# Optimization experiments

Hardware: AMD Instinct MI355X
Metric: run time of the kernel (lower is better)

The kernel has to match this reference:

```python
import jax, jax.numpy as jnp
import numpy as np

INC = 64; OUTC = 64; TS = 3; CS = 3; MAXN = 10; SIGMA = 2.0; STRIDE = 1
TAU = 0.1


def _gaussian_decay(length, max_val, sigma):
    x = np.arange(length, dtype=np.float32)
    y = max_val * np.exp(-x ** 2 / (2.0 * sigma ** 2))
    return (np.floor(y) + 1).astype(np.int64)


def _get_p_n(t_size, c_size, max_number, sigma):
    f_num = _gaussian_decay(t_size, max_number, sigma)
    c_num = _gaussian_decay(c_size, max_number, sigma)
    px, py = [], []
    for i in range(1, t_size):
        for _ in range(int(f_num[i])):
            px.append(0); py.append(i)
    for i in range(c_size):
        for _ in range(int(c_num[i])):
            px.append(i); py.append(0)
    f_number = int(f_num.sum()) - max_number - 1 if t_size > 0 else 0
    for i in range(c_size):
        for j in range(c_size):
            px.append(i); py.append(j)
    p_n = np.stack([np.array(px, np.float32), np.array(py, np.float32)], 0)  # (2, N)
    return p_n, f_number, p_n.shape[1] - f_number


def _conv(x, w, b, groups=1, pad=0):
    y = jax.lax.conv_general_dilated(
        x, w, (1, 1), [(pad, pad), (pad, pad)],
        dimension_numbers=('NCHW', 'OIHW', 'NCHW'), feature_group_count=groups)
    return y + b[None, :, None, None]


def _bilinear_sample_zeros(img, coords):
    # img (b,c,H,W); coords (b,N,h,w,2) pixel-space (x,y); zeros padding, align_corners=True
    b, c, H, W = img.shape
    x = coords[..., 0]; y = coords[..., 1]
    x0 = jnp.floor(x); y0 = jnp.floor(y)
    wx1 = x - x0; wy1 = y - y0

    def gather(yi, xi, wgt):
        valid = (xi >= 0) & (xi <= W - 1) & (yi >= 0) & (yi <= H - 1)
        xc = jnp.clip(xi, 0, W - 1).astype(jnp.int32)
        yc = jnp.clip(yi, 0, H - 1).astype(jnp.int32)
        vals = jax.vmap(lambda im, yy, xx: im[:, yy, xx])(img, yc, xc)  # (b,c,N,h,w)
        return vals * (wgt * valid.astype(img.dtype))[:, None]

    return (gather(y0, x0, (1 - wy1) * (1 - wx1)) + gather(y0, x0 + 1, (1 - wy1) * wx1)
            + gather(y0 + 1, x0, wy1 * (1 - wx1)) + gather(y0 + 1, x0 + 1, wy1 * wx1))


def setup_inputs() -> dict:
    key = jax.random.key(0)
    ks = jax.random.split(key, 12)
    p_n_np, f_num, c_num = _get_p_n(TS, CS, MAXN, SIGMA)
    N = p_n_np.shape[1]  # 52
    B, H, W = 4, 64, 64
    s = 0.05
    return {
        'x': jax.random.normal(ks[0], (B, INC, H, W), jnp.float32),
        'p_n': jnp.asarray(p_n_np),
        'dwf_w': jax.random.normal(ks[1], (INC, 1, 3, 3), jnp.float32) * s,
        'dwf_b': jnp.zeros((INC,), jnp.float32),
        'pwf_w': jax.random.normal(ks[2], (2 * f_num, INC, 1, 1), jnp.float32) * s,
        'pwf_b': jnp.zeros((2 * f_num,), jnp.float32),
        'dwc_w': jax.random.normal(ks[3], (INC, 1, 3, 3), jnp.float32) * s,
        'dwc_b': jnp.zeros((INC,), jnp.float32),
        'pwc_w': jax.random.normal(ks[4], (2 * c_num, INC, 1, 1), jnp.float32) * s,
        'pwc_b': jnp.zeros((2 * c_num,), jnp.float32),
        'dwm_w': jax.random.normal(ks[5], (INC, 1, 3, 3), jnp.float32) * s,
        'dwm_b': jnp.zeros((INC,), jnp.float32),
        'pwm_w': jax.random.normal(ks[6], (N + 1, INC, 1, 1), jnp.float32) * s,
        'pwm_b': jnp.zeros((N + 1,), jnp.float32),
        'pc_w': jax.random.normal(ks[7], (OUTC, INC, 1, 1), jnp.float32) * s,
        'pc_b': jnp.zeros((OUTC,), jnp.float32),
        'mlp_w1': jax.random.normal(ks[8], (OUTC, OUTC), jnp.float32) * s,
        'mlp_b1': jnp.zeros((OUTC,), jnp.float32),
        'mlp_w2': jax.random.normal(ks[9], (OUTC, OUTC), jnp.float32) * s,
        'mlp_b2': jnp.zeros((OUTC,), jnp.float32),
    }


def reference(x, p_n, dwf_w, dwf_b, pwf_w, pwf_b, dwc_w, dwc_b, pwc_w, pwc_b,
              dwm_w, dwm_b, pwm_w, pwm_b, pc_w, pc_b, mlp_w1, mlp_b1, mlp_w2, mlp_b2):
    b, c, H, W = x.shape
    N = p_n.shape[1]
    # learned per-pixel offsets (depthwise 3x3 + pointwise 1x1), concat f then c branch
    off_f = _conv(_conv(x, dwf_w, dwf_b, groups=c, pad=1), pwf_w, pwf_b)
    off_c = _conv(_conv(x, dwc_w, dwc_b, groups=c, pad=1), pwc_w, pwc_b)
    offset = jnp.concatenate([off_f, off_c], axis=1)  # (b, 2N, h, w)
    h, w = offset.shape[2], offset.shape[3]
    # modulation scores with learned sparsity threshold
    m = _conv(_conv(x, dwm_w, dwm_b, groups=c, pad=1), pwm_w, pwm_b)  # (b, N+1, h, w)
    sparsity = m[:, -1:]
    scores = m[:, :N]
    soft_mask = jax.nn.sigmoid((scores - sparsity) / TAU)
    mod = jax.nn.softmax(scores + jnp.log(soft_mask + 1e-10), axis=1)  # (b,N,h,w)
    # absolute sampling coordinates: base grid + fixed pattern p_n + learned offset
    dt = x.dtype
    gy, gx = jnp.meshgrid(jnp.arange(0, h * STRIDE, STRIDE, dtype=dt),
                          jnp.arange(0, w * STRIDE, STRIDE, dtype=dt), indexing='ij')
    grid = jnp.stack([gx, gy], -1)[None, None]            # (1,1,h,w,2)
    pn = p_n.T[None, :, None, None, :]                    # (1,N,1,1,2)
    off = offset.reshape(b, 2, N, h, w).transpose(0, 2, 3, 4, 1)  # (b,N,h,w,2)
    abs_c = grid + pn + off
    # normalize to [-1,1] then back to pixel space (grid_sample align_corners=True)
    nx = 2.0 * abs_c[..., 0] / (W - 1) - 1.0
    ny = 2.0 * abs_c[..., 1] / (H - 1) - 1.0
    coords = jnp.stack([(nx + 1.0) * 0.5 * (W - 1), (ny + 1.0) * 0.5 * (H - 1)], -1)
    sampled = _bilinear_sample_zeros(jax.lax.stop_gradient(x), coords)  # (b,c,N,h,w)
    agg = jnp.einsum('bcnhw,bnhw->bchw', sampled, mod)
    out = _conv(agg, pc_w, pc_b)  # 1x1 pointwise conv -> (b,outc,h,w)
    # per-pixel MLP over channels
    h1 = jax.nn.relu(jnp.einsum('bchw,dc->bdhw', out, mlp_w1) + mlp_b1[None, :, None, None])
    h2 = jnp.einsum('bchw,dc->bdhw', h1, mlp_w2) + mlp_b2[None, :, None, None]
    return h2 + x
```

## Files before the change

### kernel.cpp

```cpp
#include <hip/hip_runtime.h>
#include <hip/hip_fp16.h>
#include <cmath>

#define BB 4
#define HH 64
#define WW 64

#define OFFW  9960
#define SBW   13392
#define CMAP  15247
#define FLBC  16072
#define FLB   16073
#define POOLW 18377
#define WIN_H 0
#define TF_H  12240
#define TC_H  14800
#define TM_H  17360
#define AGG_H 34194
#define PCB_H 19920
#define H1_H  22480

typedef _Float16 f16x8 __attribute__((ext_vector_type(8)));
typedef float    f32x4 __attribute__((ext_vector_type(4)));

__global__ __launch_bounds__(256) void transpose_half(const float* __restrict__ x,
                                                      __half* __restrict__ xth) {
    int bid = blockIdx.x;
    int b = bid >> 6, y = bid & 63;
    __shared__ float tile[64][65];
    const float* xp = x + ((size_t)b * 64 * HH + y) * WW;
    #pragma unroll
    for (int k = 0; k < 16; ++k) {
        int idx = threadIdx.x + (k << 8);
        int c = idx >> 6, w = idx & 63;
        tile[c][w] = xp[(size_t)c * HH * WW + w];
    }
    __syncthreads();
    __half* op = xth + ((size_t)(b * HH + y) * WW) * 64;
    #pragma unroll
    for (int k = 0; k < 16; ++k) {
        int idx = threadIdx.x + (k << 8);
        int w = idx >> 6, c = idx & 63;
        op[(size_t)w * 64 + c] = __float2half(tile[c][w]);
    }
}

__device__ inline f32x4 tile_gemm64(const __half* PH, int actH,
                                    const float* __restrict__ W,
                                    const float* __restrict__ Bv,
                                    int m_t, int n_t, int lane) {
    const int row = m_t * 16 + (lane & 15);
    const int kg  = (lane >> 4) * 8;
    const float* wr = W + row * 64 + kg;
    float4 wa0 = *reinterpret_cast<const float4*>(wr);
    float4 wa1 = *reinterpret_cast<const float4*>(wr + 4);
    float4 wb0 = *reinterpret_cast<const float4*>(wr + 32);
    float4 wb1 = *reinterpret_cast<const float4*>(wr + 36);
    f16x8 a0, a1;
    a0[0]=(_Float16)wa0.x; a0[1]=(_Float16)wa0.y; a0[2]=(_Float16)wa0.z; a0[3]=(_Float16)wa0.w;
    a0[4]=(_Float16)wa1.x; a0[5]=(_Float16)wa1.y; a0[6]=(_Float16)wa1.z; a0[7]=(_Float16)wa1.w;
    a1[0]=(_Float16)wb0.x; a1[1]=(_Float16)wb0.y; a1[2]=(_Float16)wb0.z; a1[3]=(_Float16)wb0.w;
    a1[4]=(_Float16)wb1.x; a1[5]=(_Float16)wb1.y; a1[6]=(_Float16)wb1.z; a1[7]=(_Float16)wb1.w;
    const int px = n_t * 16 + (lane & 15);
    f16x8 b0 = *reinterpret_cast<const f16x8*>(&PH[actH + px * 80 + kg]);
    f16x8 b1 = *reinterpret_cast<const f16x8*>(&PH[actH + px * 80 + 32 + kg]);
    f32x4 d;
    const int r0 = m_t * 16 + ((lane >> 4) << 2);
    #pragma unroll
    for (int r = 0; r < 4; ++r) d[r] = Bv[r0 + r];
    d = __builtin_amdgcn_mfma_f32_16x16x32_f16(a0, b0, d, 0, 0, 0);
    d = __builtin_amdgcn_mfma_f32_16x16x32_f16(a1, b1, d, 0, 0, 0);
    return d;
}

__global__ __launch_bounds__(512, 4) void crossd_main(
    const __half* __restrict__ xth, const float* __restrict__ x,
    const float* __restrict__ p_n,
    const float* __restrict__ dwf_w, const float* __restrict__ dwf_b,
    const float* __restrict__ pwf_w, const float* __restrict__ pwf_b,
    const float* __restrict__ dwc_w, const float* __restrict__ dwc_b,
    const float* __restrict__ pwc_w, const float* __restrict__ pwc_b,
    const float* __restrict__ dwm_w, const float* __restrict__ dwm_b,
    const float* __restrict__ pwm_w, const float* __restrict__ pwm_b,
    const float* __restrict__ pc_w, const float* __restrict__ pc_b,
    const float* __restrict__ w1, const float* __restrict__ b1,
    const float* __restrict__ w2, const float* __restrict__ b2,
    float* __restrict__ out)
{
    __shared__ float P[POOLW];
    uint32_t* PU = reinterpret_cast<uint32_t*>(P);
    __half*   PH = reinterpret_cast<__half*>(P);
    const int tid  = threadIdx.x;
    const int lane = tid & 63;
    const int wv   = __builtin_amdgcn_readfirstlane(tid >> 6);
    const int bid = blockIdx.x;
    const int xh = bid & 1, y = (bid >> 1) & 63, b = bid >> 7;
    const int x0 = xh << 5;
    const int ry0 = min(max(y - 1, 0), 59);
    const __half* xbh = xth + (size_t)b * (HH * WW * 64);
    const uint2* xb2 = reinterpret_cast<const uint2*>(xbh);

    {
        for (int idx = tid; idx < 5 * 36 * 16; idx += 512) {
            int j = idx / 576;
            int rem = idx - j * 576;
            int col = rem >> 4, c4v = idx & 15;
            int gcol = min(max(x0 - 1 + col, 0), 63);
            *reinterpret_cast<uint2*>(&PH[(j * 36 + col) * 68 + c4v * 4]) =
                xb2[(((ry0 + j) << 6) + gcol) * 16 + c4v];
        }
        for (int i = tid; i < 25 * 33 + 1; i += 512) P[CMAP + i] = 0.0f;
    }
    __syncthreads();

    {
        const int c = lane;
        float wf9[9], wc9[9], wm9[9];
        #pragma unroll
        for (int k9 = 0; k9 < 9; ++k9) {
            wf9[k9] = dwf_w[c * 9 + k9];
            wc9[k9] = dwc_w[c * 9 + k9];
            wm9[k9] = dwm_w[c * 9 + k9];
        }
        const float bf = dwf_b[c], bc = dwc_b[c], bm = dwm_b[c];
        #pragma unroll
        for (int i = 0; i < 4; ++i) {
            const int pl = wv * 4 + i;
            const int pg = x0 + pl;
            float af = bf, ac = bc, am = bm;
            #pragma unroll
            for (int dy = 0; dy < 3; ++dy) {
                int yy = y + dy - 1;
                if (yy < 0 || yy >= HH) continue;
                int j = yy - ry0;
                #pragma unroll
                for (int dx = 0; dx < 3; ++dx) {
                    int xx = pg + dx - 1;
                    if (xx < 0 || xx >= WW) continue;
                    int co = xx - x0 + 1;
                    float v = __half2float(PH[(j * 36 + co) * 68 + c]);
                    int k = dy * 3 + dx;
                    af = fmaf(v, wf9[k], af);
                    ac = fmaf(v, wc9[k], ac);
                    am = fmaf(v, wm9[k], am);
                }
            }
            PH[TF_H + pl * 80 + c] = __float2half(af);
            PH[TC_H + pl * 80 + c] = __float2half(ac);
            PH[TM_H + pl * 80 + c] = __float2half(am);
        }
    }
    __syncthreads();

    {
        const int n_t = wv & 1;
        const int g   = wv >> 1;
        #pragma unroll
        for (int t = 0; t < 3; ++t) {
            const int m_t = g + t * 4;
            if (m_t < 11) {
                const float *Wb, *Bvb; int rows, actH, r0b, br;
                if (m_t < 2)      { Wb=pwf_w; Bvb=pwf_b; rows=32; actH=TF_H; r0b=m_t*16;     br=0; }
                else if (m_t < 7) { Wb=pwc_w; Bvb=pwc_b; rows=72; actH=TC_H; r0b=(m_t-2)*16; br=1; }
                else              { Wb=pwm_w; Bvb=pwm_b; rows=53; actH=TM_H; r0b=(m_t-7)*16; br=2; }
                const int rl  = min(r0b + (lane & 15), rows - 1);
                const int kg  = (lane >> 4) * 8;
                const float* wr = Wb + rl * 64 + kg;
                float4 wa0 = *reinterpret_cast<const float4*>(wr);
                float4 wa1 = *reinterpret_cast<const float4*>(wr + 4);
                float4 wb0 = *reinterpret_cast<const float4*>(wr + 32);
                float4 wb1 = *reinterpret_cast<const float4*>(wr + 36);
                f16x8 a0, a1;
                a0[0]=(_Float16)wa0.x; a0[1]=(_Float16)wa0.y; a0[2]=(_Float16)wa0.z; a0[3]=(_Float16)wa0.w;
                a0[4]=(_Float16)wa1.x; a0[5]=(_Float16)wa1.y; a0[6]=(_Float16)wa1.z; a0[7]=(_Float16)wa1.w;
                a1[0]=(_Float16)wb0.x; a1[1]=(_Float16)wb0.y; a1[2]=(_Float16)wb0.z; a1[3]=(_Float16)wb0.w;
                a1[4]=(_Float16)wb1.x; a1[5]=(_Float16)wb1.y; a1[6]=(_Float16)wb1.z; a1[7]=(_Float16)wb1.w;
                const int px = n_t * 16 + (lane & 15);
                f16x8 b0 = *reinterpret_cast<const f16x8*>(&PH[actH + px * 80 + kg]);
                f16x8 b1 = *reinterpret_cast<const f16x8*>(&PH[actH + px * 80 + 32 + kg]);
                f32x4 d;
                const int rr0 = r0b + ((lane >> 4) << 2);
                #pragma unroll
                for (int r = 0; r < 4; ++r) d[r] = Bvb[min(rr0 + r, rows - 1)];
                d = __builtin_amdgcn_mfma_f32_16x16x32_f16(a0, b0, d, 0, 0, 0);
                d = __builtin_amdgcn_mfma_f32_16x16x32_f16(a1, b1, d, 0, 0, 0);
                #pragma unroll
                for (int r = 0; r < 4; ++r) {
                    const int rb = rr0 + r;
                    if (rb < rows) {
                        const float v = d[r];
                        if (br == 2)      P[SBW + rb * 35 + px] = v;
                        else {
                            int og = (br == 0) ? rb : 32 + rb;
                            P[OFFW + og * 33 + px] = v;
                        }
                    }
                }
            }
        }
    }
    __syncthreads();

    #pragma unroll 1
    for (int i = 0; i < 4; ++i) {
        const int pl = wv * 4 + i;
        const float sp = P[SBW + 52 * 35 + pl];
        float z = -1e30f;
        if (lane < 52) {
            float s  = P[SBW + lane * 35 + pl];
            float sg = 1.0f / (1.0f + __expf(-(s - sp) * 10.0f));
            z = s + __logf(sg + 1e-10f);
        }
        float mx = z;
        #pragma unroll
        for (int d = 32; d >= 1; d >>= 1) mx = fmaxf(mx, __shfl_xor(mx, d));
        float e = (lane < 52) ? __expf(z - mx) : 0.0f;
        float sm = e;
        #pragma unroll
        for (int d = 32; d >= 1; d >>= 1) sm += __shfl_xor(sm, d);
        if (lane < 52) {
            const float mo = e / sm;
            const int pg = x0 + pl;
            float sx = (float)pg + p_n[lane]      + P[OFFW + lane * 33 + pl];
            float sy = (float)y  + p_n[52 + lane] + P[OFFW + (52 + lane) * 33 + pl];
            float x0f = floorf(sx), y0f = floorf(sy);
            float wx1 = sx - x0f, wy1 = sy - y0f;
            float wx0 = 1.0f - wx1, wy0 = 1.0f - wy1;
            int xi = (int)x0f, yi = (int)y0f;
            bool vx0 = (xi >= 0)  & (xi <= 63);
            bool vx1 = (xi >= -1) & (xi <= 62);
            bool vy0 = (yi >= 0)  & (yi <= 63);
            bool vy1 = (yi >= -1) & (yi <= 62);
            float m00 = (vy0 & vx0) ? mo * wy0 * wx0 : 0.0f;
            float m01 = (vy0 & vx1) ? mo * wy0 * wx1 : 0.0f;
            float m10 = (vy1 & vx0) ? mo * wy1 * wx0 : 0.0f;
            float m11 = (vy1 & vx1) ? mo * wy1 * wx1 : 0.0f;
            const int i0 = xi - pg + 1, j0 = yi - ry0;
            #define PUSH(m, jj, ii, gx, gy) \
                if (m != 0.0f) { \
                    if ((jj) >= 0 && (jj) <= 4 && (ii) >= 0 && (ii) <= 4) { \
                        atomicAdd(&P[CMAP + ((jj) * 5 + (ii)) * 33 + pl], m); \
                    } else { \
                        uint32_t a = (uint32_t)((gy) * 64 + (gx)); \
                        uint32_t sl = atomicAdd(&PU[FLBC], 1u); \
                        if (sl < 512u) { \
                            PU[FLB + sl * 2]     = a | ((uint32_t)pl << 16); \
                            PU[FLB + sl * 2 + 1] = __float_as_uint(m); \
                        } \
                    } \
                }
            PUSH(m00, j0,     i0,     xi,     yi);
            PUSH(m01, j0,     i0 + 1, xi + 1, yi);
            PUSH(m10, j0 + 1, i0,     xi,     yi + 1);
            PUSH(m11, j0 + 1, i0 + 1, xi + 1, yi + 1);
            #undef PUSH
        }
    }
    __syncthreads();

    {
        const int sub = lane >> 4;
        const int c4  = lane & 15;
        const int spx = wv * 4 + sub;
        const int spg = x0 + spx;
        int co[5];
        #pragma unroll
        for (int i = 0; i < 5; ++i) co[i] = min(max(spg - 1 + i, 0), 63) - x0 + 1;
        float4 agg = make_float4(0.f, 0.f, 0.f, 0.f);
        #pragma unroll
        for (int j = 0; j < 5; ++j) {
            #pragma unroll
            for (int i = 0; i < 5; ++i) {
                float w = P[CMAP + (j * 5 + i) * 33 + spx];
                uint2 u = *reinterpret_cast<const uint2*>(&PH[(j * 36 + co[i]) * 68 + c4 * 4]);
                __half2 hlo = *reinterpret_cast<const __half2*>(&u.x);
                __half2 hhi = *reinterpret_cast<const __half2*>(&u.y);
                float2 flo = __half22float2(hlo), fhi = __half22float2(hhi);
                agg.x = fmaf(w, flo.x, agg.x); agg.y = fmaf(w, flo.y, agg.y);
                agg.z = fmaf(w, fhi.x, agg.z); agg.w = fmaf(w, fhi.y, agg.w);
            }
        }
        const int cnt = min((int)PU[FLBC], 512);
        for (int e = 0; e < cnt; ++e) {
            uint32_t ea = PU[FLB + e * 2];
            float m = __uint_as_float(PU[FLB + e * 2 + 1]);
            if ((int)(ea >> 16) == spx) {
                uint2 u = xb2[(ea & 0xFFFFu) * 16 + c4];
                __half2 hlo = *reinterpret_cast<const __half2*>(&u.x);
                __half2 hhi = *reinterpret_cast<const __half2*>(&u.y);
                float2 flo = __half22float2(hlo), fhi = __half22float2(hhi);
                agg.x = fmaf(m, flo.x, agg.x); agg.y = fmaf(m, flo.y, agg.y);
                agg.z = fmaf(m, fhi.x, agg.z); agg.w = fmaf(m, fhi.y, agg.w);
            }
        }
        __half2 p0 = __floats2half2_rn(agg.x, agg.y);
        __half2 p1 = __floats2half2_rn(agg.z, agg.w);
        uint2 pk2;
        pk2.x = *reinterpret_cast<uint32_t*>(&p0);
        pk2.y = *reinterpret_cast<uint32_t*>(&p1);
        *reinterpret_cast<uint2*>(&PH[AGG_H + spx * 80 + c4 * 4]) = pk2;
    }
    __syncthreads();

    {
        f32x4 d = tile_gemm64(PH, AGG_H, pc_w, pc_b, wv >> 1, wv & 1, lane);
        const int px = (wv & 1) * 16 + (lane & 15);
        const int o0 = (wv >> 1) * 16 + ((lane >> 4) << 2);
        __half2 p0 = __floats2half2_rn(d[0], d[1]);
        __half2 p1 = __floats2half2_rn(d[2], d[3]);
        uint2 pk2;
        pk2.x = *reinterpret_cast<uint32_t*>(&p0);
        pk2.y = *reinterpret_cast<uint32_t*>(&p1);
        *reinterpret_cast<uint2*>(&PH[PCB_H + px * 80 + o0]) = pk2;
    }
    __syncthreads();

    {
        f32x4 d = tile_gemm64(PH, PCB_H, w1, b1, wv >> 1, wv & 1, lane);
        #pragma unroll
        for (int r = 0; r < 4; ++r) d[r] = fmaxf(d[r], 0.0f);
        const int px = (wv & 1) * 16 + (lane & 15);
        const int o0 = (wv >> 1) * 16 + ((lane >> 4) << 2);
        __half2 p0 = __floats2half2_rn(d[0], d[1]);
        __half2 p1 = __floats2half2_rn(d[2], d[3]);
        uint2 pk2;
        pk2.x = *reinterpret_cast<uint32_t*>(&p0);
        pk2.y = *reinterpret_cast<uint32_t*>(&p1);
        *reinterpret_cast<uint2*>(&PH[H1_H + px * 80 + o0]) = pk2;
    }
    __syncthreads();

    {
        f32x4 d = tile_gemm64(PH, H1_H, w2, b2, wv >> 1, wv & 1, lane);
        const int px = (wv & 1) * 16 + (lane & 15);
        const int o0 = (wv >> 1) * 16 + ((lane >> 4) << 2);
        #pragma unroll
        for (int r = 0; r < 4; ++r) {
            const int o = o0 + r;
            size_t idx = (((size_t)b * 64 + o) * 64 + y) * 64 + x0 + px;
            out[idx] = d[r] + x[idx];
        }
    }
}

extern "C" void kernel_launch(void* const* d_in, const int* in_sizes, int n_in,
                              void* d_out, int out_size, void* d_ws, size_t ws_size,
                              hipStream_t stream) {
    const float* x     = (const float*)d_in[0];
    const float* p_n   = (const float*)d_in[1];
    const float* dwf_w = (const float*)d_in[2];
    const float* dwf_b = (const float*)d_in[3];
    const float* pwf_w = (const float*)d_in[4];
    const float* pwf_b = (const float*)d_in[5];
    const float* dwc_w = (const float*)d_in[6];
    const float* dwc_b = (const float*)d_in[7];
    const float* pwc_w = (const float*)d_in[8];
    const float* pwc_b = (const float*)d_in[9];
    const float* dwm_w = (const float*)d_in[10];
    const float* dwm_b = (const float*)d_in[11];
    const float* pwm_w = (const float*)d_in[12];
    const float* pwm_b = (const float*)d_in[13];
    const float* pc_w  = (const float*)d_in[14];
    const float* pc_b  = (const float*)d_in[15];
    const float* w1    = (const float*)d_in[16];
    const float* b1    = (const float*)d_in[17];
    const float* w2    = (const float*)d_in[18];
    const float* b2    = (const float*)d_in[19];

    __half* xth = (__half*)d_ws;
    float* outp = (float*)d_out;

    hipLaunchKernelGGL(transpose_half, dim3(BB * HH), dim3(256), 0, stream, x, xth);
    hipLaunchKernelGGL(crossd_main, dim3(BB * HH * 2), dim3(512), 0, stream,
                       xth, x, p_n,
                       dwf_w, dwf_b, pwf_w, pwf_b,
                       dwc_w, dwc_b, pwc_w, pwc_b,
                       dwm_w, dwm_b, pwm_w, pwm_b,
                       pc_w, pc_b, w1, b1, w2, b2, outp);
}
```

Before: 48.83 us.

## Drop separate transpose kernel; load NCHW fp32 input directly into shared tile

Removes the pre-pass kernel that transposed x into a channels-last fp16 workspace. The main kernel now reads the NCHW fp32 input directly, converting to fp16 as it fills the shared halo tile, and the fallback far-sample path reads four strided fp32 channel values. This saves one kernel launch and a full write and read of the transposed tensor. In exchange the halo load makes scalar 4-byte reads with less vectorisation, and far samples now hit four separate cache lines per pixel instead of one 8-byte chunk.

```diff
diff --git a/kernel.cpp b/kernel.cpp
--- a/kernel.cpp
+++ b/kernel.cpp
@@ -22,28 +22,6 @@
 
 typedef _Float16 f16x8 __attribute__((ext_vector_type(8)));
 typedef float    f32x4 __attribute__((ext_vector_type(4)));
-
-__global__ __launch_bounds__(256) void transpose_half(const float* __restrict__ x,
-                                                      __half* __restrict__ xth) {
-    int bid = blockIdx.x;
-    int b = bid >> 6, y = bid & 63;
-    __shared__ float tile[64][65];
-    const float* xp = x + ((size_t)b * 64 * HH + y) * WW;
-    #pragma unroll
-    for (int k = 0; k < 16; ++k) {
-        int idx = threadIdx.x + (k << 8);
-        int c = idx >> 6, w = idx & 63;
-        tile[c][w] = xp[(size_t)c * HH * WW + w];
-    }
-    __syncthreads();
-    __half* op = xth + ((size_t)(b * HH + y) * WW) * 64;
-    #pragma unroll
-    for (int k = 0; k < 16; ++k) {
-        int idx = threadIdx.x + (k << 8);
-        int w = idx >> 6, c = idx & 63;
-        op[(size_t)w * 64 + c] = __float2half(tile[c][w]);
-    }
-}
 
 __device__ inline f32x4 tile_gemm64(const __half* PH, int actH,
                                     const float* __restrict__ W,
@@ -74,7 +52,7 @@
 }
 
 __global__ __launch_bounds__(512, 4) void crossd_main(
-    const __half* __restrict__ xth, const float* __restrict__ x,
+    const float* __restrict__ x,
     const float* __restrict__ p_n,
     const float* __restrict__ dwf_w, const float* __restrict__ dwf_b,
     const float* __restrict__ pwf_w, const float* __restrict__ pwf_b,
@@ -97,17 +75,17 @@
     const int xh = bid & 1, y = (bid >> 1) & 63, b = bid >> 7;
     const int x0 = xh << 5;
     const int ry0 = min(max(y - 1, 0), 59);
-    const __half* xbh = xth + (size_t)b * (HH * WW * 64);
-    const uint2* xb2 = reinterpret_cast<const uint2*>(xbh);
-
-    {
-        for (int idx = tid; idx < 5 * 36 * 16; idx += 512) {
-            int j = idx / 576;
-            int rem = idx - j * 576;
-            int col = rem >> 4, c4v = idx & 15;
+    const float* xb = x + (size_t)b * (64 * HH * WW);
+
+    {
+        for (int idx = tid; idx < 5 * 64 * 36; idx += 512) {
+            int j   = idx / (64 * 36);
+            int rem = idx - j * (64 * 36);
+            int c   = rem / 36;
+            int col = rem - c * 36;
             int gcol = min(max(x0 - 1 + col, 0), 63);
-            *reinterpret_cast<uint2*>(&PH[(j * 36 + col) * 68 + c4v * 4]) =
-                xb2[(((ry0 + j) << 6) + gcol) * 16 + c4v];
+            float v = xb[((size_t)c * HH + (ry0 + j)) * WW + gcol];
+            PH[(j * 36 + col) * 68 + c] = __float2half(v);
         }
         for (int i = tid; i < 25 * 33 + 1; i += 512) P[CMAP + i] = 0.0f;
     }
@@ -285,12 +263,13 @@
             uint32_t ea = PU[FLB + e * 2];
             float m = __uint_as_float(PU[FLB + e * 2 + 1]);
             if ((int)(ea >> 16) == spx) {
-                uint2 u = xb2[(ea & 0xFFFFu) * 16 + c4];
-                __half2 hlo = *reinterpret_cast<const __half2*>(&u.x);
-                __half2 hhi = *reinterpret_cast<const __half2*>(&u.y);
-                float2 flo = __half22float2(hlo), fhi = __half22float2(hhi);
-                agg.x = fmaf(m, flo.x, agg.x); agg.y = fmaf(m, flo.y, agg.y);
-                agg.z = fmaf(m, fhi.x, agg.z); agg.w = fmaf(m, fhi.y, agg.w);
+                int gy = (int)((ea & 0xFFFFu) >> 6), gx = (int)(ea & 63u);
+                float v0 = xb[((size_t)(c4 * 4 + 0) * HH + gy) * WW + gx];
+                float v1 = xb[((size_t)(c4 * 4 + 1) * HH + gy) * WW + gx];
+                float v2 = xb[((size_t)(c4 * 4 + 2) * HH + gy) * WW + gx];
+                float v3 = xb[((size_t)(c4 * 4 + 3) * HH + gy) * WW + gx];
+                agg.x = fmaf(m, v0, agg.x); agg.y = fmaf(m, v1, agg.y);
+                agg.z = fmaf(m, v2, agg.z); agg.w = fmaf(m, v3, agg.w);
             }
         }
         __half2 p0 = __floats2half2_rn(agg.x, agg.y);
@@ -367,12 +346,10 @@
     const float* w2    = (const float*)d_in[18];
     const float* b2    = (const float*)d_in[19];
 
-    __half* xth = (__half*)d_ws;
     float* outp = (float*)d_out;
 
-    hipLaunchKernelGGL(transpose_half, dim3(BB * HH), dim3(256), 0, stream, x, xth);
     hipLaunchKernelGGL(crossd_main, dim3(BB * HH * 2), dim3(512), 0, stream,
-                       xth, x, p_n,
+                       x, p_n,
                        dwf_w, dwf_b, pwf_w, pwf_b,
                        dwc_w, dwc_b, pwc_w, pwc_b,
                        dwm_w, dwm_b, pwm_w, pwm_b,
```

Result: faster. 46.07 us (median of 2 runs) (-5.7%).
